# Performance work log

Hardware: AMD Instinct MI355X
Metric: run time of the kernel (lower is better)

## Reference

```python
import jax, jax.numpy as jnp
import numpy as np

JITTER = 0.1

def se_kernel(X, X2, length_scale):
    # K[i,j] = exp(-||x_i - x2_j||^2 / length_scale^2)   (no 1/2 factor, as in source)
    Xs = X / length_scale
    X2s = X2 / length_scale
    d2 = (jnp.sum(Xs * Xs, axis=1)[:, None]
          - 2.0 * Xs @ X2s.T
          + jnp.sum(X2s * X2s, axis=1)[None, :])
    return jnp.exp(-d2)

def kron(A, B):
    # kronecker(A, B) as in source: einsum 'ab,cd->acbd' then reshape
    return jnp.einsum('ab,cd->acbd', A, B).reshape(A.shape[0] * B.shape[0], A.shape[1] * B.shape[1])

def setup_inputs() -> dict:
    key = jax.random.key(0)
    ks = jax.random.split(key, 5)
    return {
        'space_coordinates': jax.random.normal(ks[0], (150, 3), dtype=jnp.float32),
        'time_coordinates': jax.random.normal(ks[1], (40, 1), dtype=jnp.float32),
        'stData': jax.random.normal(ks[2], (150, 40), dtype=jnp.float32),
        'test_space_coordinates': jax.random.normal(ks[3], (200, 3), dtype=jnp.float32),
        'test_time_coordinates': jax.random.normal(ks[4], (30, 1), dtype=jnp.float32),
        'log_latlong_length_scale': jnp.log(jnp.asarray(1.0, dtype=jnp.float32)),
        'log_elevation_length_scale': jnp.log(jnp.asarray(1.0, dtype=jnp.float32)),
        'log_time_length_scale': jnp.log(jnp.asarray(0.25, dtype=jnp.float32)),
        'log_noise_variance': jnp.log(jnp.asarray(0.1, dtype=jnp.float32)),
        'log_signal_variance': jnp.log(jnp.asarray(1.0, dtype=jnp.float32)),
    }

def reference(space_coordinates, time_coordinates, stData,
              test_space_coordinates, test_time_coordinates,
              log_latlong_length_scale, log_elevation_length_scale,
              log_time_length_scale, log_noise_variance, log_signal_variance):
    ll = jnp.exp(log_latlong_length_scale)
    le = jnp.exp(log_elevation_length_scale)
    lt = jnp.exp(log_time_length_scale)
    Ns = space_coordinates.shape[0]
    Nt = time_coordinates.shape[0]

    # ---- update(): build sigma_inverse and alpha via Kronecker eigendecomposition ----
    spatial_K = (se_kernel(space_coordinates[:, 0:2], space_coordinates[:, 0:2], ll)
                 * se_kernel(space_coordinates[:, 2:3], space_coordinates[:, 2:3], le)
                 + JITTER * jnp.eye(Ns, dtype=space_coordinates.dtype))
    temporal_K = (se_kernel(time_coordinates, time_coordinates, lt)
                  + JITTER * jnp.eye(Nt, dtype=time_coordinates.dtype))
    ws, Vs = jnp.linalg.eigh(spatial_K)
    wt, Vt = jnp.linalg.eigh(temporal_K)
    V = kron(Vt, Vs)                                   # [N, N], N = Nt*Ns
    w = jnp.einsum('a,b->ab', wt, ws).reshape(-1)      # eigenvalues of kron kernel
    inv = 1.0 / (w + jnp.exp(log_noise_variance))
    sigma_inverse = (V * inv[None, :]) @ V.T           # V diag(inv) V^T
    alpha = sigma_inverse @ stData.T.reshape(-1, 1)    # [N, 1]

    # ---- forward ----
    test_spatial = (se_kernel(test_space_coordinates[:, 0:2], space_coordinates[:, 0:2], ll)
                    * se_kernel(test_space_coordinates[:, 2:3], space_coordinates[:, 2:3], le))
    test_temporal = se_kernel(test_time_coordinates, time_coordinates, lt)
    Kst = kron(test_temporal, test_spatial)            # [M, N], M = Mt*Ms
    yPred = Kst @ alpha                                # [M, 1]
    # fused row-wise quadratic form: diag(Kst sigma_inverse Kst^T)
    yVar = jnp.exp(log_signal_variance) - jnp.sum((Kst @ sigma_inverse) * Kst, axis=1)
    Mt = test_time_coordinates.shape[0]
    Ms = test_space_coordinates.shape[0]
    yPred = yPred.reshape(Mt, Ms).T                    # [Ms, Mt]
    yVar = yVar.reshape(Mt, Ms).T                      # [Ms, Mt]
    return (yPred, yVar)
```

## Files before the change

kernel.cpp:

```cpp
#include <hip/hip_runtime.h>
#include <math.h>

#define NS 150
#define LDW 152
#define NPACK 11848
#define NT 40
#define MS 200
#define MT 30
#define N_SWEEPS 6
#define ROUNDS (N_SWEEPS*(NT-1))
#define JITTER 0.1f

#define OFF_MP    0
#define OFF_PR    47392
#define OFF_INVS  49824
#define OFF_DVS   49840
#define OFF_SCS   50448
#define OFF_TSCS  52256
#define OFF_QV    54656
#define OFF_RV    55456
#define OFF_GV    56256
#define OFF_ACOL  56856
#define OFF_WTJ   56976
#define SMEM_BYTES 56992
#define OFF_A2    0
#define OFF_VTS   13120
#define OFF_PRM   20160
#define OFF_TCS   21440

__device__ __forceinline__ int rs_off(int r) {
    int g = r >> 2, rm = r & 3;
    return LDW * r - 8 * g * (g - 1) - 4 * rm * g;
}

__device__ __forceinline__ void jac_params(const float (*A)[NT+1], float4* dst,
                                           int i, int rr) {
    int i0 = i, i1 = NT - 1 - i;
    int p = (i0 == 0) ? 0 : ((i0 - 1 + rr) % (NT - 1)) + 1;
    int q = ((i1 - 1 + rr) % (NT - 1)) + 1;
    if (p > q) { int tsw = p; p = q; q = tsw; }
    float app = A[p][p], aqq = A[q][q], apq = A[p][q];
    float c, s;
    if (apq == 0.0f) { c = 1.0f; s = 0.0f; }
    else {
        float tau = (aqq - app) / (2.0f * apq);
        float tt = ((tau >= 0.0f) ? 1.0f : -1.0f) / (fabsf(tau) + sqrtf(1.0f + tau*tau));
        c = rsqrtf(1.0f + tt*tt);
        s = tt * c;
    }
    dst[i] = make_float4(c, s, __int_as_float(p), __int_as_float(q));
}

__global__ void __launch_bounds__(256, 1) gp_block(
        const float* __restrict__ sc,  const float* __restrict__ tc,
        const float* __restrict__ st,  const float* __restrict__ tsc,
        const float* __restrict__ ttc,
        const float* __restrict__ lll, const float* __restrict__ lle,
        const float* __restrict__ llt, const float* __restrict__ lnv,
        const float* __restrict__ lsv, float* __restrict__ out) {
    __shared__ __align__(16) char smem[SMEM_BYTES];
    int j = blockIdx.x, tid = threadIdx.x;

    auto A2   = (float (*)[NT][NT+1])(smem + OFF_A2);
    auto Vts  = (float (*)[44])(smem + OFF_VTS);
    auto prm  = (float4 (*)[NT/2])(smem + OFF_PRM);
    float* tcs  = (float*)(smem + OFF_TCS);
    float* gv   = (float*)(smem + OFF_GV);
    float* Acol = (float*)(smem + OFF_ACOL);
    float* wtjs = (float*)(smem + OFF_WTJ);

    float ilt2 = expf(-2.0f * llt[0]);
    if (tid < NT) tcs[tid] = tc[tid];
    __syncthreads();
    for (int idx = tid; idx < NT*NT; idx += 256) {
        int i = idx / NT, jj = idx - i*NT;
        float dt = tcs[i] - tcs[jj];
        float v = expf(-dt*dt*ilt2);
        if (i == jj) v += JITTER;
        A2[0][i][jj] = v;
    }
    for (int idx = tid; idx < NT*44; idx += 256) {
        int jr = idx / 44, k = idx - jr*44;
        Vts[jr][k] = (jr == k) ? 1.0f : 0.0f;
    }
    __syncthreads();
    int wave = tid >> 6, lane = tid & 63;
    for (int rd = 0; rd < ROUNDS; ++rd) {
        int cur = rd & 1, nxt = cur ^ 1;
        float4* wp = prm[wave];
        if (lane < NT/2) jac_params(A2[cur], wp, lane, rd % (NT - 1));
        __builtin_amdgcn_wave_barrier();
        for (int t = tid; t < 600; t += 256) {
            if (t < 400) {
                int bi = t / 20, bj = t - bi*20;
                float4 Pi = wp[bi], Pj = wp[bj];
                int pi = __float_as_int(Pi.z), qi = __float_as_int(Pi.w);
                int pj = __float_as_int(Pj.z), qj = __float_as_int(Pj.w);
                float ci = Pi.x, si = Pi.y, cj = Pj.x, sj = Pj.y;
                float a00 = A2[cur][pi][pj], a01 = A2[cur][pi][qj];
                float a10 = A2[cur][qi][pj], a11 = A2[cur][qi][qj];
                float b00 = ci*a00 - si*a10, b01 = ci*a01 - si*a11;
                float b10 = si*a00 + ci*a10, b11 = si*a01 + ci*a11;
                A2[nxt][pi][pj] = cj*b00 - sj*b01; A2[nxt][pi][qj] = sj*b00 + cj*b01;
                A2[nxt][qi][pj] = cj*b10 - sj*b11; A2[nxt][qi][qj] = sj*b10 + cj*b11;
            } else {
                int u2 = t - 400;
                int pr = u2 / 10, ch = (u2 - pr*10) << 2;
                float4 P = wp[pr];
                int pj = __float_as_int(P.z), qj = __float_as_int(P.w);
                float c = P.x, s = P.y;
                float4 vp = *(float4*)&Vts[pj][ch];
                float4 vq = *(float4*)&Vts[qj][ch];
                float4 np, nq;
                np.x = c*vp.x - s*vq.x; nq.x = s*vp.x + c*vq.x;
                np.y = c*vp.y - s*vq.y; nq.y = s*vp.y + c*vq.y;
                np.z = c*vp.z - s*vq.z; nq.z = s*vp.z + c*vq.z;
                np.w = c*vp.w - s*vq.w; nq.w = s*vp.w + c*vq.w;
                *(float4*)&Vts[pj][ch] = np;
                *(float4*)&Vts[qj][ch] = nq;
            }
        }
        __syncthreads();
    }
    const int fin = ROUNDS & 1;
    if (tid == 0) wtjs[0] = A2[fin][j][j];
    for (int s = tid; s < NS; s += 256) {
        const float4* va = (const float4*)&Vts[j][0];
        const float4* sa = (const float4*)&st[s*NT];
        float acc = 0.0f;
        #pragma unroll
        for (int c4 = 0; c4 < NT/4; ++c4) {
            float4 a = va[c4], b = sa[c4];
            acc += a.x*b.x + a.y*b.y + a.z*b.z + a.w*b.w;
        }
        gv[s] = acc;
    }
    if (tid < MT) {
        float ttv = ttc[tid];
        float acc = 0.0f;
        for (int t = 0; t < NT; ++t) {
            float dt = ttv - tcs[t];
            acc += expf(-dt*dt*ilt2) * Vts[j][t];
        }
        Acol[tid] = acc;
    }
    __syncthreads();

    float* Mp   = (float*)(smem + OFF_MP);
    auto   Pr   = (float (*)[LDW])(smem + OFF_PR);
    float* invs = (float*)(smem + OFF_INVS);
    float* dvs  = (float*)(smem + OFF_DVS);
    float* scs  = (float*)(smem + OFF_SCS);
    float* tscs = (float*)(smem + OFF_TSCS);
    float* qv   = (float*)(smem + OFF_QV);
    float* Rv   = (float*)(smem + OFF_RV);
    float wtj = wtjs[0];
    float nv = expf(lnv[0]);
    float ill2 = expf(-2.0f * lll[0]);
    float ile2 = expf(-2.0f * lle[0]);
    for (int t = tid; t < NS*3; t += 256) scs[t] = sc[t];
    for (int t = tid; t < MS*3; t += 256) tscs[t] = tsc[t];
    __syncthreads();
    for (int idx = tid; idx < NS*LDW; idx += 256) {
        int r = idx / LDW, c = idx - r*LDW;
        int rbase = r & ~3;
        if (c < rbase) continue;
        float v;
        if (c < NS) {
            float d0 = scs[r*3+0] - scs[c*3+0];
            float d1 = scs[r*3+1] - scs[c*3+1];
            float d2 = scs[r*3+2] - scs[c*3+2];
            v = wtj * expf(-((d0*d0 + d1*d1)*ill2 + d2*d2*ile2));
            if (c == r) v += wtj * JITTER + nv;
        } else if (c == NS) {
            v = gv[r];
        } else {
            v = 0.0f;
        }
        Mp[rs_off(r) + c - rbase] = v;
    }
    __syncthreads();
    for (int k0 = 0; k0 < NS - 1; k0 += 4) {
        int P = NS - k0; if (P > 4) P = 4;
        int W4 = (LDW - k0) >> 2;
        if (tid < W4) {
            int o0 = rs_off(k0);
            int o1 = (P > 1) ? rs_off(k0+1) : o0;
            int o2 = (P > 2) ? rs_off(k0+2) : o0;
            int o3 = (P > 3) ? rs_off(k0+3) : o0;
            float b00 = Mp[o0+0];
            float b01 = (P>1)? Mp[o0+1] : 0.f;
            float b02 = (P>2)? Mp[o0+2] : 0.f;
            float b03 = (P>3)? Mp[o0+3] : 0.f;
            float b11 = (P>1)? Mp[o1+1] : 1.f;
            float b12 = (P>2)? Mp[o1+2] : 0.f;
            float b13 = (P>3)? Mp[o1+3] : 0.f;
            float b22 = (P>2)? Mp[o2+2] : 1.f;
            float b23 = (P>3)? Mp[o2+3] : 0.f;
            float b33 = (P>3)? Mp[o3+3] : 1.f;
            float i0 = 1.f/b00;
            float l10 = b01*i0, l20 = b02*i0, l30 = b03*i0;
            float c11 = b11 - l10*b01;
            float i1 = 1.f/c11;
            float c12 = b12 - l10*b02, c13 = b13 - l10*b03;
            float l21 = c12*i1, l31 = c13*i1;
            float c22 = b22 - l20*b02 - l21*c12;
            float i2 = 1.f/c22;
            float c23 = b23 - l20*b03 - l21*c13;
            float l32 = c23*i2;
            float c33 = b33 - l30*b03 - l31*c13 - l32*c23;
            float i3 = 1.f/c33;
            int C = tid << 2;
            float4 z = make_float4(0,0,0,0);
            float4 m0 = *(float4*)&Mp[o0 + C];
            float4 m1 = (P>1)? *(float4*)&Mp[o1 + C] : z;
            float4 m2 = (P>2)? *(float4*)&Mp[o2 + C] : z;
            float4 m3 = (P>3)? *(float4*)&Mp[o3 + C] : z;
            m1.x -= l10*m0.x; m1.y -= l10*m0.y; m1.z -= l10*m0.z; m1.w -= l10*m0.w;
            m2.x -= l20*m0.x + l21*m1.x; m2.y -= l20*m0.y + l21*m1.y;
            m2.z -= l20*m0.z + l21*m1.z; m2.w -= l20*m0.w + l21*m1.w;
            m3.x -= l30*m0.x + l31*m1.x + l32*m2.x;
            m3.y -= l30*m0.y + l31*m1.y + l32*m2.y;
            m3.z -= l30*m0.z + l31*m1.z + l32*m2.z;
            m3.w -= l30*m0.w + l31*m1.w + l32*m2.w;
            *(float4*)&Pr[0][C] = m0;
            *(float4*)&Pr[1][C] = m1;
            *(float4*)&Pr[2][C] = m2;
            *(float4*)&Pr[3][C] = m3;
            if (tid == 0) { invs[0]=i0; invs[1]=i1; invs[2]=i2; invs[3]=i3; }
        }
        __syncthreads();
        float iv0 = invs[0], iv1 = invs[1], iv2 = invs[2], iv3 = invs[3];
        for (int r = k0 + 1 + tid; r < NS; r += 256) {
            int rc = r - k0;
            int E = rc < P ? rc : P;
            float f0 = Pr[0][rc] * iv0;
            float f1 = (E > 1) ? Pr[1][rc] * iv1 : 0.f;
            float f2 = (E > 2) ? Pr[2][rc] * iv2 : 0.f;
            float f3 = (E > 3) ? Pr[3][rc] * iv3 : 0.f;
            int rbase = r & ~3;
            int ro = rs_off(r) - rbase;
            for (int C = rbase; C < LDW; C += 4) {
                int pc = C - k0;
                float4 v  = *(float4*)&Mp[ro + C];
                float4 p0 = *(float4*)&Pr[0][pc];
                float4 p1 = *(float4*)&Pr[1][pc];
                float4 p2 = *(float4*)&Pr[2][pc];
                float4 p3 = *(float4*)&Pr[3][pc];
                v.x -= f0*p0.x + f1*p1.x + f2*p2.x + f3*p3.x;
                v.y -= f0*p0.y + f1*p1.y + f2*p2.y + f3*p3.y;
                v.z -= f0*p0.z + f1*p1.z + f2*p2.z + f3*p3.z;
                v.w -= f0*p0.w + f1*p1.w + f2*p2.w + f3*p3.w;
                *(float4*)&Mp[ro + C] = v;
            }
        }
        __syncthreads();
    }
    for (int r = tid; r < NS; r += 256)
        dvs[r] = rsqrtf(Mp[rs_off(r) + r - (r & ~3)]);
    __syncthreads();
    for (int idx = tid; idx < NS*LDW; idx += 256) {
        int r = idx / LDW, c = idx - r*LDW;
        int rbase = r & ~3;
        if (c < rbase) continue;
        int t = rs_off(r) + c - rbase;
        float dvr = dvs[r];
        if (c == r) Mp[t] = dvr;
        else if (c > r) Mp[t] *= dvr;
    }
    __syncthreads();
    if (tid < MS) {
        float tx = tscs[tid*3+0], ty = tscs[tid*3+1], tz = tscs[tid*3+2];
        float u[LDW];
        #pragma unroll
        for (int k = 0; k < NS; ++k) {
            float d0 = tx - scs[k*3+0];
            float d1 = ty - scs[k*3+1];
            float d2 = tz - scs[k*3+2];
            u[k] = expf(-((d0*d0 + d1*d1)*ill2 + d2*d2*ile2));
        }
        u[150] = 0.0f; u[151] = 0.0f;
        float qa = 0.0f, ra = 0.0f;
        #pragma unroll
        for (int k = 0; k < NS; ++k) {
            const int base = rs_off(k) - (k & ~3);
            float uk = u[k] * Mp[base + k];
            qa += uk * uk;
            ra += uk * Mp[base + 150];
            const int kp = k + 1;
            const int ka = (kp + 3) & ~3;
            #pragma unroll
            for (int t = kp; t < ((ka < NS) ? ka : NS); ++t)
                u[t] -= Mp[base + t] * uk;
            #pragma unroll
            for (int t = ka; t < NS; t += 4) {
                float4 w = *(const float4*)&Mp[base + t];
                u[t+0] -= w.x * uk; u[t+1] -= w.y * uk;
                u[t+2] -= w.z * uk; u[t+3] -= w.w * uk;
            }
        }
        qv[tid] = qa;
        Rv[tid] = ra;
    }
    __syncthreads();

    float sigv = expf(lsv[0]);
    for (int idx = tid; idx < MS*MT; idx += 256) {
        int is = idx / MT, it = idx - is*MT;
        float a = Acol[it];
        atomicAdd(&out[idx], a * Rv[is]);
        float c2 = -a * a * qv[is];
        if (j == 0) c2 += sigv;
        atomicAdd(&out[MS*MT + idx], c2);
    }
}

extern "C" void kernel_launch(void* const* d_in, const int* in_sizes, int n_in,
                              void* d_out, int out_size, void* d_ws, size_t ws_size,
                              hipStream_t stream) {
    const float* sc  = (const float*)d_in[0];
    const float* tc  = (const float*)d_in[1];
    const float* st  = (const float*)d_in[2];
    const float* tsc = (const float*)d_in[3];
    const float* ttc = (const float*)d_in[4];
    const float* lll = (const float*)d_in[5];
    const float* lle = (const float*)d_in[6];
    const float* llt = (const float*)d_in[7];
    const float* lnv = (const float*)d_in[8];
    const float* lsv = (const float*)d_in[9];
    float* out = (float*)d_out;

    hipMemsetAsync(out, 0, (size_t)out_size * sizeof(float), stream);
    hipLaunchKernelGGL(gp_block, dim3(NT), dim3(256), 0, stream,
                       sc, tc, st, tsc, ttc, lll, lle, llt, lnv, lsv, out);
}
```

Measured before the change: 508.5 us.

## Use 8-row panels in block Cholesky, 512 threads, hoist coordinate loads

The blocked in-shared-memory LDL/Cholesky factorization now eliminates 8 pivot rows per step instead of 4. This halves the number of panel steps and barriers and reuses each loaded trailing element across more pivots. The block size doubles to 512 threads and the coordinate loads move to the start of the kernel, overlapping them with the Jacobi setup. The tradeoffs are heavier per-thread register use for the 8x8 panel factor and more shared-memory traffic in the panel row; idle waves during the serial Jacobi phase may also add barrier cost.

```diff
diff --git a/kernel.cpp b/kernel.cpp
--- a/kernel.cpp
+++ b/kernel.cpp
@@ -10,23 +10,24 @@
 #define N_SWEEPS 6
 #define ROUNDS (N_SWEEPS*(NT-1))
 #define JITTER 0.1f
+#define NTHR 512
 
 #define OFF_MP    0
 #define OFF_PR    47392
-#define OFF_INVS  49824
-#define OFF_DVS   49840
-#define OFF_SCS   50448
-#define OFF_TSCS  52256
-#define OFF_QV    54656
-#define OFF_RV    55456
-#define OFF_GV    56256
-#define OFF_ACOL  56856
-#define OFF_WTJ   56976
-#define SMEM_BYTES 56992
+#define OFF_INVS  52256
+#define OFF_DVS   52288
+#define OFF_SCS   52896
+#define OFF_TSCS  54704
+#define OFF_QV    57104
+#define OFF_RV    57904
+#define OFF_GV    58704
+#define OFF_ACOL  59304
+#define OFF_WTJ   59424
+#define SMEM_BYTES 59440
 #define OFF_A2    0
 #define OFF_VTS   13120
 #define OFF_PRM   20160
-#define OFF_TCS   21440
+#define OFF_TCS   22720
 
 __device__ __forceinline__ int rs_off(int r) {
     int g = r >> 2, rm = r & 3;
@@ -51,7 +52,7 @@
     dst[i] = make_float4(c, s, __int_as_float(p), __int_as_float(q));
 }
 
-__global__ void __launch_bounds__(256, 1) gp_block(
+__global__ void __launch_bounds__(NTHR, 1) gp_block(
         const float* __restrict__ sc,  const float* __restrict__ tc,
         const float* __restrict__ st,  const float* __restrict__ tsc,
         const float* __restrict__ ttc,
@@ -68,18 +69,22 @@
     float* gv   = (float*)(smem + OFF_GV);
     float* Acol = (float*)(smem + OFF_ACOL);
     float* wtjs = (float*)(smem + OFF_WTJ);
+    float* scs  = (float*)(smem + OFF_SCS);
+    float* tscs = (float*)(smem + OFF_TSCS);
 
     float ilt2 = expf(-2.0f * llt[0]);
     if (tid < NT) tcs[tid] = tc[tid];
-    __syncthreads();
-    for (int idx = tid; idx < NT*NT; idx += 256) {
+    for (int t = tid; t < NS*3; t += NTHR) scs[t] = sc[t];
+    for (int t = tid; t < MS*3; t += NTHR) tscs[t] = tsc[t];
+    __syncthreads();
+    for (int idx = tid; idx < NT*NT; idx += NTHR) {
         int i = idx / NT, jj = idx - i*NT;
         float dt = tcs[i] - tcs[jj];
         float v = expf(-dt*dt*ilt2);
         if (i == jj) v += JITTER;
         A2[0][i][jj] = v;
     }
-    for (int idx = tid; idx < NT*44; idx += 256) {
+    for (int idx = tid; idx < NT*44; idx += NTHR) {
         int jr = idx / 44, k = idx - jr*44;
         Vts[jr][k] = (jr == k) ? 1.0f : 0.0f;
     }
@@ -90,7 +95,7 @@
         float4* wp = prm[wave];
         if (lane < NT/2) jac_params(A2[cur], wp, lane, rd % (NT - 1));
         __builtin_amdgcn_wave_barrier();
-        for (int t = tid; t < 600; t += 256) {
+        for (int t = tid; t < 600; t += NTHR) {
             if (t < 400) {
                 int bi = t / 20, bj = t - bi*20;
                 float4 Pi = wp[bi], Pj = wp[bj];
@@ -124,7 +129,7 @@
     }
     const int fin = ROUNDS & 1;
     if (tid == 0) wtjs[0] = A2[fin][j][j];
-    for (int s = tid; s < NS; s += 256) {
+    for (int s = tid; s < NS; s += NTHR) {
         const float4* va = (const float4*)&Vts[j][0];
         const float4* sa = (const float4*)&st[s*NT];
         float acc = 0.0f;
@@ -150,18 +155,13 @@
     auto   Pr   = (float (*)[LDW])(smem + OFF_PR);
     float* invs = (float*)(smem + OFF_INVS);
     float* dvs  = (float*)(smem + OFF_DVS);
-    float* scs  = (float*)(smem + OFF_SCS);
-    float* tscs = (float*)(smem + OFF_TSCS);
     float* qv   = (float*)(smem + OFF_QV);
     float* Rv   = (float*)(smem + OFF_RV);
     float wtj = wtjs[0];
     float nv = expf(lnv[0]);
     float ill2 = expf(-2.0f * lll[0]);
     float ile2 = expf(-2.0f * lle[0]);
-    for (int t = tid; t < NS*3; t += 256) scs[t] = sc[t];
-    for (int t = tid; t < MS*3; t += 256) tscs[t] = tsc[t];
-    __syncthreads();
-    for (int idx = tid; idx < NS*LDW; idx += 256) {
+    for (int idx = tid; idx < NS*LDW; idx += NTHR) {
         int r = idx / LDW, c = idx - r*LDW;
         int rbase = r & ~3;
         if (c < rbase) continue;
@@ -180,86 +180,84 @@
         Mp[rs_off(r) + c - rbase] = v;
     }
     __syncthreads();
-    for (int k0 = 0; k0 < NS - 1; k0 += 4) {
-        int P = NS - k0; if (P > 4) P = 4;
+    for (int k0 = 0; k0 < NS - 1; k0 += 8) {
+        int P = NS - k0; if (P > 8) P = 8;
         int W4 = (LDW - k0) >> 2;
         if (tid < W4) {
-            int o0 = rs_off(k0);
-            int o1 = (P > 1) ? rs_off(k0+1) : o0;
-            int o2 = (P > 2) ? rs_off(k0+2) : o0;
-            int o3 = (P > 3) ? rs_off(k0+3) : o0;
-            float b00 = Mp[o0+0];
-            float b01 = (P>1)? Mp[o0+1] : 0.f;
-            float b02 = (P>2)? Mp[o0+2] : 0.f;
-            float b03 = (P>3)? Mp[o0+3] : 0.f;
-            float b11 = (P>1)? Mp[o1+1] : 1.f;
-            float b12 = (P>2)? Mp[o1+2] : 0.f;
-            float b13 = (P>3)? Mp[o1+3] : 0.f;
-            float b22 = (P>2)? Mp[o2+2] : 1.f;
-            float b23 = (P>3)? Mp[o2+3] : 0.f;
-            float b33 = (P>3)? Mp[o3+3] : 1.f;
-            float i0 = 1.f/b00;
-            float l10 = b01*i0, l20 = b02*i0, l30 = b03*i0;
-            float c11 = b11 - l10*b01;
-            float i1 = 1.f/c11;
-            float c12 = b12 - l10*b02, c13 = b13 - l10*b03;
-            float l21 = c12*i1, l31 = c13*i1;
-            float c22 = b22 - l20*b02 - l21*c12;
-            float i2 = 1.f/c22;
-            float c23 = b23 - l20*b03 - l21*c13;
-            float l32 = c23*i2;
-            float c33 = b33 - l30*b03 - l31*c13 - l32*c23;
-            float i3 = 1.f/c33;
+            int off[8];
+            #pragma unroll
+            for (int i = 0; i < 8; ++i)
+                off[i] = (i < P) ? (rs_off(k0 + i) - ((i >= 4) ? 4 : 0)) : 0;
+            float Bm[8][8];
+            #pragma unroll
+            for (int i = 0; i < 8; ++i) {
+                #pragma unroll
+                for (int c = 0; c < 8; ++c)
+                    Bm[i][c] = (i < P && c >= i) ? Mp[off[i] + c]
+                                                 : ((c == i) ? 1.0f : 0.0f);
+            }
+            float Lf[8][8]; float iv[8];
+            #pragma unroll
+            for (int k = 0; k < 8; ++k) {
+                iv[k] = 1.0f / Bm[k][k];
+                #pragma unroll
+                for (int i = k + 1; i < 8; ++i) {
+                    float l = Bm[k][i] * iv[k];
+                    Lf[i][k] = l;
+                    #pragma unroll
+                    for (int c = i; c < 8; ++c) Bm[i][c] -= l * Bm[k][c];
+                }
+            }
+            if (tid == 0) {
+                #pragma unroll
+                for (int i = 0; i < 8; ++i) invs[i] = iv[i];
+            }
             int C = tid << 2;
-            float4 z = make_float4(0,0,0,0);
-            float4 m0 = *(float4*)&Mp[o0 + C];
-            float4 m1 = (P>1)? *(float4*)&Mp[o1 + C] : z;
-            float4 m2 = (P>2)? *(float4*)&Mp[o2 + C] : z;
-            float4 m3 = (P>3)? *(float4*)&Mp[o3 + C] : z;
-            m1.x -= l10*m0.x; m1.y -= l10*m0.y; m1.z -= l10*m0.z; m1.w -= l10*m0.w;
-            m2.x -= l20*m0.x + l21*m1.x; m2.y -= l20*m0.y + l21*m1.y;
-            m2.z -= l20*m0.z + l21*m1.z; m2.w -= l20*m0.w + l21*m1.w;
-            m3.x -= l30*m0.x + l31*m1.x + l32*m2.x;
-            m3.y -= l30*m0.y + l31*m1.y + l32*m2.y;
-            m3.z -= l30*m0.z + l31*m1.z + l32*m2.z;
-            m3.w -= l30*m0.w + l31*m1.w + l32*m2.w;
-            *(float4*)&Pr[0][C] = m0;
-            *(float4*)&Pr[1][C] = m1;
-            *(float4*)&Pr[2][C] = m2;
-            *(float4*)&Pr[3][C] = m3;
-            if (tid == 0) { invs[0]=i0; invs[1]=i1; invs[2]=i2; invs[3]=i3; }
+            float4 m[8];
+            #pragma unroll
+            for (int i = 0; i < 8; ++i) {
+                bool ok = (i < P) && (i < 4 || C >= 4);
+                m[i] = ok ? *(float4*)&Mp[off[i] + C] : make_float4(0,0,0,0);
+            }
+            #pragma unroll
+            for (int i = 1; i < 8; ++i) {
+                #pragma unroll
+                for (int k = 0; k < i; ++k) {
+                    float l = Lf[i][k];
+                    m[i].x -= l*m[k].x; m[i].y -= l*m[k].y;
+                    m[i].z -= l*m[k].z; m[i].w -= l*m[k].w;
+                }
+            }
+            #pragma unroll
+            for (int i = 0; i < 8; ++i) *(float4*)&Pr[i][C] = m[i];
         }
         __syncthreads();
-        float iv0 = invs[0], iv1 = invs[1], iv2 = invs[2], iv3 = invs[3];
-        for (int r = k0 + 1 + tid; r < NS; r += 256) {
+        for (int r = k0 + 1 + tid; r < NS; r += NTHR) {
             int rc = r - k0;
-            int E = rc < P ? rc : P;
-            float f0 = Pr[0][rc] * iv0;
-            float f1 = (E > 1) ? Pr[1][rc] * iv1 : 0.f;
-            float f2 = (E > 2) ? Pr[2][rc] * iv2 : 0.f;
-            float f3 = (E > 3) ? Pr[3][rc] * iv3 : 0.f;
+            float f[8];
+            #pragma unroll
+            for (int i = 0; i < 8; ++i)
+                f[i] = (rc > i && i < P) ? Pr[i][rc] * invs[i] : 0.0f;
             int rbase = r & ~3;
             int ro = rs_off(r) - rbase;
             for (int C = rbase; C < LDW; C += 4) {
                 int pc = C - k0;
-                float4 v  = *(float4*)&Mp[ro + C];
-                float4 p0 = *(float4*)&Pr[0][pc];
-                float4 p1 = *(float4*)&Pr[1][pc];
-                float4 p2 = *(float4*)&Pr[2][pc];
-                float4 p3 = *(float4*)&Pr[3][pc];
-                v.x -= f0*p0.x + f1*p1.x + f2*p2.x + f3*p3.x;
-                v.y -= f0*p0.y + f1*p1.y + f2*p2.y + f3*p3.y;
-                v.z -= f0*p0.z + f1*p1.z + f2*p2.z + f3*p3.z;
-                v.w -= f0*p0.w + f1*p1.w + f2*p2.w + f3*p3.w;
+                float4 v = *(float4*)&Mp[ro + C];
+                #pragma unroll
+                for (int i = 0; i < 8; ++i) {
+                    float4 p = *(float4*)&Pr[i][pc];
+                    v.x -= f[i]*p.x; v.y -= f[i]*p.y;
+                    v.z -= f[i]*p.z; v.w -= f[i]*p.w;
+                }
                 *(float4*)&Mp[ro + C] = v;
             }
         }
         __syncthreads();
     }
-    for (int r = tid; r < NS; r += 256)
+    for (int r = tid; r < NS; r += NTHR)
         dvs[r] = rsqrtf(Mp[rs_off(r) + r - (r & ~3)]);
     __syncthreads();
-    for (int idx = tid; idx < NS*LDW; idx += 256) {
+    for (int idx = tid; idx < NS*LDW; idx += NTHR) {
         int r = idx / LDW, c = idx - r*LDW;
         int rbase = r & ~3;
         if (c < rbase) continue;
@@ -305,7 +303,7 @@
     __syncthreads();
 
     float sigv = expf(lsv[0]);
-    for (int idx = tid; idx < MS*MT; idx += 256) {
+    for (int idx = tid; idx < MS*MT; idx += NTHR) {
         int is = idx / MT, it = idx - is*MT;
         float a = Acol[it];
         atomicAdd(&out[idx], a * Rv[is]);
@@ -331,6 +329,6 @@
     float* out = (float*)d_out;
 
     hipMemsetAsync(out, 0, (size_t)out_size * sizeof(float), stream);
-    hipLaunchKernelGGL(gp_block, dim3(NT), dim3(256), 0, stream,
+    hipLaunchKernelGGL(gp_block, dim3(NT), dim3(NTHR), 0, stream,
                        sc, tc, st, tsc, ttc, lll, lle, llt, lnv, lsv, out);
 }
```

After: 418.4 us, median of 3. 17.7% less time.
